# Optimization experiments

Hardware: AMD Instinct MI355X
Metric: run time of the kernel (lower is better)

The kernel has to match this reference:

```python
import jax, jax.numpy as jnp
import numpy as np

B, T, C = 8, 2048, 1024
HEAD = 64
BLOCK = 2048  # block_size == max_size == ramp_size


def setup_inputs() -> dict:
    key = jax.random.key(0)
    kx, kq, kk, kv = jax.random.split(key, 4)
    x = jax.random.normal(kx, (B, T, C), dtype=jnp.float32)
    # torch Linear(n_embd, head_size, bias=False): store as (C, HEAD) for x @ W
    s = 1.0 / np.sqrt(C)
    Wq = jax.random.uniform(kq, (C, HEAD), dtype=jnp.float32, minval=-s, maxval=s)
    Wk = jax.random.uniform(kk, (C, HEAD), dtype=jnp.float32, minval=-s, maxval=s)
    Wv = jax.random.uniform(kv, (C, HEAD), dtype=jnp.float32, minval=-s, maxval=s)
    # adaptive_span current_val parameter, shape (1,1,1), init 0
    current_val = jnp.zeros((1, 1, 1), dtype=jnp.float32)
    return {"x": x, "Wq": Wq, "Wk": Wk, "Wv": Wv, "current_val": current_val}


def reference(x, Wq, Wk, Wv, current_val):
    Bb, Tt, Cc = x.shape
    q = x @ Wq  # (B,T,H)
    k = x @ Wk
    v = x @ Wv
    scale = 1.0 / jnp.sqrt(jnp.asarray(HEAD, dtype=x.dtype))
    scores = jnp.einsum('bth,bsh->bts', q, k) * scale  # (B,T,T)
    causal = jnp.tril(jnp.ones((Tt, Tt), dtype=bool))
    scores = jnp.where(causal, scores, -jnp.inf)
    w = jax.nn.softmax(scores, axis=-1)
    # adaptive span post-softmax mask (T == max_size here, so no slicing)
    template = jnp.linspace(1.0 - BLOCK, 0.0, BLOCK, dtype=x.dtype)  # (T,)
    span = template + current_val * BLOCK  # (1,1,T)
    span = jnp.clip(span / BLOCK + 1.0, 0.0, 1.0)
    w = w * span
    w = w / (w.sum(-1, keepdims=True) + 1e-8)
    # dropout p=0 (eval) -> identity
    out = jnp.einsum('bts,bsh->bth', w, v)  # (B,T,H)
    return out
```

## Files before the change

kernel.cpp:

```cpp
#include <hip/hip_runtime.h>
#include <hip/hip_bf16.h>

#define BSZ 8
#define T 2048
#define C 1024
#define H 64
#define M (BSZ*T)

typedef __attribute__((ext_vector_type(4))) float f32x4;
typedef __attribute__((ext_vector_type(8))) short bf16x8;
typedef __attribute__((ext_vector_type(4))) short s16x4;
typedef __attribute__((ext_vector_type(8))) short s16x8;

static __device__ __forceinline__ short f2bf(float f) {
  union { float f; unsigned u; } c; c.f = f;
  unsigned u = c.u;
  u = (u + 0x7fffu + ((u >> 16) & 1u)) >> 16;
  return (short)u;
}

__global__ __launch_bounds__(256) void k_wt(const float* __restrict__ Wq,
                                            const float* __restrict__ Wk,
                                            const float* __restrict__ Wv,
                                            short* __restrict__ wt) {
  int idx = blockIdx.x * 256 + threadIdx.x;
  int c = idx & (C - 1);
  int n = idx >> 10;
  int w = n >> 6;
  int h = n & (H - 1);
  const float* W = (w == 0) ? Wq : (w == 1) ? Wk : Wv;
  wt[idx] = f2bf(W[c * H + h]);
}

__global__ __launch_bounds__(256) void k_qkv(const float* __restrict__ x,
                                             const short* __restrict__ wt,
                                             short* __restrict__ qb,
                                             short* __restrict__ kb,
                                             short* __restrict__ vt) {
  __shared__ short xs[2][32 * 64];
  __shared__ short wl[2][192 * 64];
  const int tid = threadIdx.x;
  const int m0 = blockIdx.x * 32;
  const int lane = tid & 63;
  const int wid = tid >> 6;
  const int g16 = lane >> 4, l16 = lane & 15;
  const int row0 = (wid & 1) * 16;
  const int nc0 = (wid >> 1) * 96;

  f32x4 acc[6];
  #pragma unroll
  for (int i = 0; i < 6; ++i) acc[i] = (f32x4){0.f, 0.f, 0.f, 0.f};

  const int xr = tid >> 4;
  const int xc4 = (tid & 15) * 4;
  const int xsw = xc4 ^ ((xr & 7) << 3);
  const int wr = tid >> 3;
  const int wc8 = (tid & 7) * 8;
  const int wsw = wc8 ^ ((wr & 7) << 3);
  const int fsw = (l16 & 7) << 3;

  float4 xA0, xA1, xB0, xB1;
  s16x8 wA0, wA1, wA2, wA3, wA4, wA5;
  s16x8 wB0, wB1, wB2, wB3, wB4, wB5;

#define QKV_LOAD(S, kc) do { \
    x##S##0 = *(const float4*)&x[(size_t)(m0 + xr) * C + (kc) + xc4]; \
    x##S##1 = *(const float4*)&x[(size_t)(m0 + xr + 16) * C + (kc) + xc4]; \
    w##S##0 = *(const s16x8*)&wt[(wr +   0) * C + (kc) + wc8]; \
    w##S##1 = *(const s16x8*)&wt[(wr +  32) * C + (kc) + wc8]; \
    w##S##2 = *(const s16x8*)&wt[(wr +  64) * C + (kc) + wc8]; \
    w##S##3 = *(const s16x8*)&wt[(wr +  96) * C + (kc) + wc8]; \
    w##S##4 = *(const s16x8*)&wt[(wr + 128) * C + (kc) + wc8]; \
    w##S##5 = *(const s16x8*)&wt[(wr + 160) * C + (kc) + wc8]; \
  } while (0)

#define QKV_STORE(S, buf) do { \
    s16x4 h0 = { f2bf((x##S##0).x), f2bf((x##S##0).y), f2bf((x##S##0).z), f2bf((x##S##0).w) }; \
    s16x4 h1 = { f2bf((x##S##1).x), f2bf((x##S##1).y), f2bf((x##S##1).z), f2bf((x##S##1).w) }; \
    *(s16x4*)&xs[buf][xr * 64 + xsw] = h0; \
    *(s16x4*)&xs[buf][(xr + 16) * 64 + xsw] = h1; \
    *(s16x8*)&wl[buf][(wr +   0) * 64 + wsw] = w##S##0; \
    *(s16x8*)&wl[buf][(wr +  32) * 64 + wsw] = w##S##1; \
    *(s16x8*)&wl[buf][(wr +  64) * 64 + wsw] = w##S##2; \
    *(s16x8*)&wl[buf][(wr +  96) * 64 + wsw] = w##S##3; \
    *(s16x8*)&wl[buf][(wr + 128) * 64 + wsw] = w##S##4; \
    *(s16x8*)&wl[buf][(wr + 160) * 64 + wsw] = w##S##5; \
  } while (0)

#define QKV_COMPUTE(buf) do { \
    _Pragma("unroll") \
    for (int ks = 0; ks < 2; ++ks) { \
      bf16x8 a = *(const bf16x8*)&xs[buf][(row0 + l16) * 64 + ((ks * 32 + g16 * 8) ^ fsw)]; \
      _Pragma("unroll") \
      for (int nt = 0; nt < 6; ++nt) { \
        bf16x8 bfr = *(const bf16x8*)&wl[buf][(nc0 + nt * 16 + l16) * 64 + ((ks * 32 + g16 * 8) ^ fsw)]; \
        acc[nt] = __builtin_amdgcn_mfma_f32_16x16x32_bf16(a, bfr, acc[nt], 0, 0, 0); \
      } \
    } \
  } while (0)

  QKV_LOAD(A, 0);
  QKV_STORE(A, 0);
  QKV_LOAD(B, 64);
  __syncthreads();

  #pragma unroll 1
  for (int ii = 0; ii < 8; ++ii) {
    if (ii < 7) QKV_LOAD(A, (2 * ii + 2) * 64);
    QKV_STORE(B, 1);
    QKV_COMPUTE(0);
    __syncthreads();
    if (ii < 7) {
      QKV_LOAD(B, (2 * ii + 3) * 64);
      QKV_STORE(A, 0);
    }
    QKV_COMPUTE(1);
    if (ii < 7) __syncthreads();
  }
#undef QKV_LOAD
#undef QKV_STORE
#undef QKV_COMPUTE

  const int r0 = row0 + g16 * 4;
  #pragma unroll
  for (int nt = 0; nt < 6; ++nt) {
    const int nglob = nc0 + nt * 16;
    const int which = nglob >> 6;
    const int col = (nglob & 63) + l16;
    #pragma unroll
    for (int j = 0; j < 4; ++j) {
      const int tg = m0 + r0 + j;
      const short val = f2bf(acc[nt][j]);
      if (which == 0)      qb[tg * H + col] = val;
      else if (which == 1) kb[tg * H + col] = val;
      else {
        const int b = tg >> 11, tl = tg & (T - 1);
        vt[((b << 6) + col) * T + tl] = val;
      }
    }
  }
}

__global__ __launch_bounds__(512, 4) void k_attn(const short* __restrict__ qb,
                                                 const short* __restrict__ kb,
                                                 const short* __restrict__ vt,
                                                 const float* __restrict__ cvp,
                                                 float* __restrict__ out) {
  __shared__ __align__(16) char smem[34816];
  short (*plds)[2][16][40] = (short (*)[2][16][40])smem;
  float (*Ow)[16][68]      = (float (*)[16][68])smem;
  __shared__ float mw[8][16];
  __shared__ float Lw[8][16];
  const int pid = blockIdx.x;
  const int b = pid & 7;
  const int pr = pid >> 3;
  const int tA = pr, tB = 127 - pr;
  const int q0A = tA << 4, q0B = tB << 4;
  const int nitA = (q0A + 47) >> 5;
  const int nitB = (q0B + 47) >> 5;
  const int NT = nitA + nitB;
  int wA = (8 * nitA + (NT >> 1)) / NT;
  wA = wA < 1 ? 1 : (wA > 7 ? 7 : wA);

  const int tid = threadIdx.x;
  const int wid = tid >> 6;
  const int lane = tid & 63;
  const int g16 = lane >> 4, l16 = lane & 15;
  const float cv = cvp[0];
  const float SCL = 0.125f * 1.44269504f;

  const bool onA = (wid < wA);
  const int q0 = onA ? q0A : q0B;
  const int nitW = onA ? nitA : nitB;
  const int nwt = onA ? wA : 8 - wA;
  const int wg = onA ? wid : wid - wA;
  const int npw = (nitW + nwt - 1) / nwt;
  const int lo = wg * npw;
  const int hi = (lo + npw < nitW) ? lo + npw : nitW;

  const short* qp = qb + ((size_t)(b << 11) + q0 + l16) * H + g16 * 8;
  bf16x8 qf0 = *(const bf16x8*)qp;
  bf16x8 qf1 = *(const bf16x8*)(qp + 32);
  const int qg = q0 + l16;

  float m = -3e38f, L = 0.f;
  f32x4 O[4];
  #pragma unroll
  for (int t4 = 0; t4 < 4; ++t4) O[t4] = (f32x4){0.f, 0.f, 0.f, 0.f};

  if (lo < hi) {
    const short* kp = kb + ((size_t)(b << 11) + lo * 32 + l16) * H + g16 * 8;
    const short* vp = vt + ((size_t)(b << 6) + l16) * T + lo * 32 + g16 * 8;
    bf16x8 kc0 = *(const bf16x8*)kp;
    bf16x8 kc1 = *(const bf16x8*)(kp + 32);
    bf16x8 kc2 = *(const bf16x8*)(kp + 16 * H);
    bf16x8 kc3 = *(const bf16x8*)(kp + 16 * H + 32);
    kp += 32 * H;

    for (int it = lo; it < hi; ++it) {
      bf16x8 kn0, kn1, kn2, kn3;
      const bool more = (it + 1 < hi);
      if (more) {
        kn0 = *(const bf16x8*)kp;
        kn1 = *(const bf16x8*)(kp + 32);
        kn2 = *(const bf16x8*)(kp + 16 * H);
        kn3 = *(const bf16x8*)(kp + 16 * H + 32);
      }
      bf16x8 v0 = *(const bf16x8*)vp;
      bf16x8 v1 = *(const bf16x8*)(vp + 16 * T);
      bf16x8 v2 = *(const bf16x8*)(vp + 32 * T);
      bf16x8 v3 = *(const bf16x8*)(vp + 48 * T);

      f32x4 s0 = {0.f,0.f,0.f,0.f}, s1 = {0.f,0.f,0.f,0.f};
      s0 = __builtin_amdgcn_mfma_f32_16x16x32_bf16(kc0, qf0, s0, 0, 0, 0);
      s0 = __builtin_amdgcn_mfma_f32_16x16x32_bf16(kc1, qf1, s0, 0, 0, 0);
      s1 = __builtin_amdgcn_mfma_f32_16x16x32_bf16(kc2, qf0, s1, 0, 0, 0);
      s1 = __builtin_amdgcn_mfma_f32_16x16x32_bf16(kc3, qf1, s1, 0, 0, 0);

      const int kv0 = it << 5;
      const int kvb = kv0 + g16 * 4;
      const bool diag = (kv0 + 31 > q0);
      float sv[8];
      if (diag) {
        #pragma unroll
        for (int r = 0; r < 8; ++r) {
          const int kvg = kvb + ((r >> 2) << 4) + (r & 3);
          const float s = ((r < 4) ? s0[r] : s1[r - 4]) * SCL;
          sv[r] = (kvg <= qg) ? s : -1e30f;
        }
      } else {
        #pragma unroll
        for (int r = 0; r < 8; ++r)
          sv[r] = ((r < 4) ? s0[r] : s1[r - 4]) * SCL;
      }

      float pmax = fmaxf(fmaxf(fmaxf(sv[0], sv[1]), fmaxf(sv[2], sv[3])),
                         fmaxf(fmaxf(sv[4], sv[5]), fmaxf(sv[6], sv[7])));
      if (!__all(pmax <= m + 7.f)) {
        float v = pmax;
        v = fmaxf(v, __shfl_xor(v, 16, 64));
        v = fmaxf(v, __shfl_xor(v, 32, 64));
        const float mn = fmaxf(m, v);
        const float al = exp2f(m - mn);
        m = mn;
        L *= al;
        #pragma unroll
        for (int t4 = 0; t4 < 4; ++t4) O[t4] *= al;
      }

      float p[8];
      #pragma unroll
      for (int r = 0; r < 8; ++r) {
        const int kvg = kvb + ((r >> 2) << 4) + (r & 3);
        const float sp = fminf(fmaxf((float)(kvg + 1) * (1.f / 2048.f) + cv, 0.f), 1.f);
        p[r] = exp2f(sv[r] - m) * sp;
      }
      if (diag) {
        #pragma unroll
        for (int r = 0; r < 8; ++r) {
          const int kvg = kvb + ((r >> 2) << 4) + (r & 3);
          p[r] = (kvg <= qg) ? p[r] : 0.f;
        }
      }
      L += ((p[0] + p[1]) + (p[2] + p[3])) + ((p[4] + p[5]) + (p[6] + p[7]));

      short (*pl)[40] = plds[wid][it & 1];
      #pragma unroll
      for (int r = 0; r < 8; r += 2) {
        union { float f; unsigned u; } a0, a1;
        a0.f = p[r]; a1.f = p[r + 1];
        const unsigned pk = (a0.u >> 16) | (a1.u & 0xffff0000u);
        *(unsigned*)&pl[l16][((r >> 2) << 4) + g16 * 4 + (r & 3)] = pk;
      }
      bf16x8 pa = *(const bf16x8*)&pl[l16][g16 * 8];
      O[0] = __builtin_amdgcn_mfma_f32_16x16x32_bf16(v0, pa, O[0], 0, 0, 0);
      O[1] = __builtin_amdgcn_mfma_f32_16x16x32_bf16(v1, pa, O[1], 0, 0, 0);
      O[2] = __builtin_amdgcn_mfma_f32_16x16x32_bf16(v2, pa, O[2], 0, 0, 0);
      O[3] = __builtin_amdgcn_mfma_f32_16x16x32_bf16(v3, pa, O[3], 0, 0, 0);

      if (more) { kc0 = kn0; kc1 = kn1; kc2 = kn2; kc3 = kn3; }
      kp += 32 * H;
      vp += 32;
    }
  }

  __syncthreads();

  float Lr = L;
  Lr += __shfl_xor(Lr, 16, 64);
  Lr += __shfl_xor(Lr, 32, 64);
  if (g16 == 0) { mw[wid][l16] = m; Lw[wid][l16] = Lr; }
  #pragma unroll
  for (int t4 = 0; t4 < 4; ++t4)
    *(f32x4*)&Ow[wid][l16][t4 * 16 + g16 * 4] = O[t4];
  __syncthreads();

  {
    const int r32 = tid >> 4;
    const int c4 = (tid & 15) << 2;
    const bool rowA = (r32 < 16);
    const int r = rowA ? r32 : r32 - 16;
    const int w0 = rowA ? 0 : wA;
    const int w1 = rowA ? wA : 8;
    const int q0r = rowA ? q0A : q0B;
    float Mx = -3e38f;
    for (int w = w0; w < w1; ++w) Mx = fmaxf(Mx, mw[w][r]);
    float Ls = 0.f;
    f32x4 o = (f32x4){0.f, 0.f, 0.f, 0.f};
    for (int w = w0; w < w1; ++w) {
      const float fw = exp2f(mw[w][r] - Mx);
      Ls += Lw[w][r] * fw;
      f32x4 ow = *(const f32x4*)&Ow[w][r][c4];
      o += ow * fw;
    }
    o *= 1.f / (Ls + 1e-30f);
    *(f32x4*)&out[(size_t)((b << 11) + q0r + r) * H + c4] = o;
  }
}

extern "C" void kernel_launch(void* const* d_in, const int* in_sizes, int n_in,
                              void* d_out, int out_size, void* d_ws, size_t ws_size,
                              hipStream_t stream) {
  const float* x  = (const float*)d_in[0];
  const float* Wq = (const float*)d_in[1];
  const float* Wk = (const float*)d_in[2];
  const float* Wv = (const float*)d_in[3];
  const float* cv = (const float*)d_in[4];
  float* out = (float*)d_out;

  char* ws = (char*)d_ws;
  short* qb = (short*)(ws);
  short* kb = (short*)(ws + (size_t)M * H * 2);
  short* vt = (short*)(ws + (size_t)2 * M * H * 2);
  short* wt = (short*)(ws + (size_t)3 * M * H * 2);

  hipLaunchKernelGGL(k_wt, dim3(3 * H * C / 256), dim3(256), 0, stream, Wq, Wk, Wv, wt);
  hipLaunchKernelGGL(k_qkv, dim3(M / 32), dim3(256), 0, stream, x, wt, qb, kb, vt);
  hipLaunchKernelGGL(k_attn, dim3(BSZ * T / 32), dim3(512), 0, stream, qb, kb, vt, cv, out);
}
```

Before: 63.40 us.

## Software-pipeline QK MFMA one step ahead and exchange P via ds_bpermute

The attention loop is restructured so the QK^T MFMAs for the next key block run while the current block's softmax and PV MFMAs execute. K loads are double-buffered two steps ahead using an unrolled ping-pong lambda. The P tile is now moved from the score layout to the MFMA operand layout with ds_bpermute lane shuffles instead of an LDS round-trip, which also removes the shared P buffer and a __syncthreads. Launch bounds drop from 4 to 2 waves-per-EU, allowing more registers for the extra live state at the cost of possible occupancy.

```diff
diff --git a/kernel.cpp b/kernel.cpp
--- a/kernel.cpp
+++ b/kernel.cpp
@@ -141,21 +141,18 @@
   }
 }
 
-__global__ __launch_bounds__(512, 4) void k_attn(const short* __restrict__ qb,
+__global__ __launch_bounds__(512, 2) void k_attn(const short* __restrict__ qb,
                                                  const short* __restrict__ kb,
                                                  const short* __restrict__ vt,
                                                  const float* __restrict__ cvp,
                                                  float* __restrict__ out) {
-  __shared__ __align__(16) char smem[34816];
-  short (*plds)[2][16][40] = (short (*)[2][16][40])smem;
-  float (*Ow)[16][68]      = (float (*)[16][68])smem;
+  __shared__ float Ow[8][16][68];
   __shared__ float mw[8][16];
   __shared__ float Lw[8][16];
   const int pid = blockIdx.x;
   const int b = pid & 7;
   const int pr = pid >> 3;
-  const int tA = pr, tB = 127 - pr;
-  const int q0A = tA << 4, q0B = tB << 4;
+  const int q0A = pr << 4, q0B = (127 - pr) << 4;
   const int nitA = (q0A + 47) >> 5;
   const int nitB = (q0B + 47) >> 5;
   const int NT = nitA + nitB;
@@ -183,6 +180,11 @@
   bf16x8 qf1 = *(const bf16x8*)(qp + 32);
   const int qg = q0 + l16;
 
+  const int gsel = (g16 & 1) << 5;
+  const int addrA = (gsel + l16) << 2;
+  const int addrB = (gsel + 16 + l16) << 2;
+  const bool ghi = (g16 >= 2);
+
   float m = -3e38f, L = 0.f;
   f32x4 O[4];
   #pragma unroll
@@ -191,31 +193,46 @@
   if (lo < hi) {
     const short* kp = kb + ((size_t)(b << 11) + lo * 32 + l16) * H + g16 * 8;
     const short* vp = vt + ((size_t)(b << 6) + l16) * T + lo * 32 + g16 * 8;
-    bf16x8 kc0 = *(const bf16x8*)kp;
-    bf16x8 kc1 = *(const bf16x8*)(kp + 32);
-    bf16x8 kc2 = *(const bf16x8*)(kp + 16 * H);
-    bf16x8 kc3 = *(const bf16x8*)(kp + 16 * H + 32);
+    bf16x8 kA0 = *(const bf16x8*)kp;
+    bf16x8 kA1 = *(const bf16x8*)(kp + 32);
+    bf16x8 kA2 = *(const bf16x8*)(kp + 16 * H);
+    bf16x8 kA3 = *(const bf16x8*)(kp + 16 * H + 32);
     kp += 32 * H;
-
-    for (int it = lo; it < hi; ++it) {
-      bf16x8 kn0, kn1, kn2, kn3;
-      const bool more = (it + 1 < hi);
-      if (more) {
-        kn0 = *(const bf16x8*)kp;
-        kn1 = *(const bf16x8*)(kp + 32);
-        kn2 = *(const bf16x8*)(kp + 16 * H);
-        kn3 = *(const bf16x8*)(kp + 16 * H + 32);
-      }
+    bf16x8 kB0 = kA0, kB1 = kA1, kB2 = kA2, kB3 = kA3;
+    if (lo + 1 < hi) {
+      kB0 = *(const bf16x8*)kp;
+      kB1 = *(const bf16x8*)(kp + 32);
+      kB2 = *(const bf16x8*)(kp + 16 * H);
+      kB3 = *(const bf16x8*)(kp + 16 * H + 32);
+      kp += 32 * H;
+    }
+    f32x4 s0c = {0.f,0.f,0.f,0.f}, s1c = {0.f,0.f,0.f,0.f};
+    s0c = __builtin_amdgcn_mfma_f32_16x16x32_bf16(kA0, qf0, s0c, 0, 0, 0);
+    s0c = __builtin_amdgcn_mfma_f32_16x16x32_bf16(kA1, qf1, s0c, 0, 0, 0);
+    s1c = __builtin_amdgcn_mfma_f32_16x16x32_bf16(kA2, qf0, s1c, 0, 0, 0);
+    s1c = __builtin_amdgcn_mfma_f32_16x16x32_bf16(kA3, qf1, s1c, 0, 0, 0);
+
+    auto astep = [&](int it,
+                     bf16x8 kn0, bf16x8 kn1, bf16x8 kn2, bf16x8 kn3,
+                     bf16x8& kl0, bf16x8& kl1, bf16x8& kl2, bf16x8& kl3) {
       bf16x8 v0 = *(const bf16x8*)vp;
       bf16x8 v1 = *(const bf16x8*)(vp + 16 * T);
       bf16x8 v2 = *(const bf16x8*)(vp + 32 * T);
       bf16x8 v3 = *(const bf16x8*)(vp + 48 * T);
-
-      f32x4 s0 = {0.f,0.f,0.f,0.f}, s1 = {0.f,0.f,0.f,0.f};
-      s0 = __builtin_amdgcn_mfma_f32_16x16x32_bf16(kc0, qf0, s0, 0, 0, 0);
-      s0 = __builtin_amdgcn_mfma_f32_16x16x32_bf16(kc1, qf1, s0, 0, 0, 0);
-      s1 = __builtin_amdgcn_mfma_f32_16x16x32_bf16(kc2, qf0, s1, 0, 0, 0);
-      s1 = __builtin_amdgcn_mfma_f32_16x16x32_bf16(kc3, qf1, s1, 0, 0, 0);
+      if (it + 2 < hi) {
+        kl0 = *(const bf16x8*)kp;
+        kl1 = *(const bf16x8*)(kp + 32);
+        kl2 = *(const bf16x8*)(kp + 16 * H);
+        kl3 = *(const bf16x8*)(kp + 16 * H + 32);
+        kp += 32 * H;
+      }
+      f32x4 n0 = {0.f,0.f,0.f,0.f}, n1 = {0.f,0.f,0.f,0.f};
+      if (it + 1 < hi) {
+        n0 = __builtin_amdgcn_mfma_f32_16x16x32_bf16(kn0, qf0, n0, 0, 0, 0);
+        n0 = __builtin_amdgcn_mfma_f32_16x16x32_bf16(kn1, qf1, n0, 0, 0, 0);
+        n1 = __builtin_amdgcn_mfma_f32_16x16x32_bf16(kn2, qf0, n1, 0, 0, 0);
+        n1 = __builtin_amdgcn_mfma_f32_16x16x32_bf16(kn3, qf1, n1, 0, 0, 0);
+      }
 
       const int kv0 = it << 5;
       const int kvb = kv0 + g16 * 4;
@@ -225,15 +242,14 @@
         #pragma unroll
         for (int r = 0; r < 8; ++r) {
           const int kvg = kvb + ((r >> 2) << 4) + (r & 3);
-          const float s = ((r < 4) ? s0[r] : s1[r - 4]) * SCL;
+          const float s = ((r < 4) ? s0c[r] : s1c[r - 4]) * SCL;
           sv[r] = (kvg <= qg) ? s : -1e30f;
         }
       } else {
         #pragma unroll
         for (int r = 0; r < 8; ++r)
-          sv[r] = ((r < 4) ? s0[r] : s1[r - 4]) * SCL;
-      }
-
+          sv[r] = ((r < 4) ? s0c[r] : s1c[r - 4]) * SCL;
+      }
       float pmax = fmaxf(fmaxf(fmaxf(sv[0], sv[1]), fmaxf(sv[2], sv[3])),
                          fmaxf(fmaxf(sv[4], sv[5]), fmaxf(sv[6], sv[7])));
       if (!__all(pmax <= m + 7.f)) {
@@ -247,7 +263,6 @@
         #pragma unroll
         for (int t4 = 0; t4 < 4; ++t4) O[t4] *= al;
       }
-
       float p[8];
       #pragma unroll
       for (int r = 0; r < 8; ++r) {
@@ -264,27 +279,43 @@
       }
       L += ((p[0] + p[1]) + (p[2] + p[3])) + ((p[4] + p[5]) + (p[6] + p[7]));
 
-      short (*pl)[40] = plds[wid][it & 1];
-      #pragma unroll
-      for (int r = 0; r < 8; r += 2) {
-        union { float f; unsigned u; } a0, a1;
-        a0.f = p[r]; a1.f = p[r + 1];
-        const unsigned pk = (a0.u >> 16) | (a1.u & 0xffff0000u);
-        *(unsigned*)&pl[l16][((r >> 2) << 4) + g16 * 4 + (r & 3)] = pk;
-      }
-      bf16x8 pa = *(const bf16x8*)&pl[l16][g16 * 8];
+      union { float f; unsigned u; } a0, a1;
+      unsigned d0, d1, d2, d3;
+      a0.f = p[0]; a1.f = p[1]; d0 = (a0.u >> 16) | (a1.u & 0xffff0000u);
+      a0.f = p[2]; a1.f = p[3]; d1 = (a0.u >> 16) | (a1.u & 0xffff0000u);
+      a0.f = p[4]; a1.f = p[5]; d2 = (a0.u >> 16) | (a1.u & 0xffff0000u);
+      a0.f = p[6]; a1.f = p[7]; d3 = (a0.u >> 16) | (a1.u & 0xffff0000u);
+      const int lo0 = __builtin_amdgcn_ds_bpermute(addrA, (int)d0);
+      const int lo1 = __builtin_amdgcn_ds_bpermute(addrA, (int)d1);
+      const int lo2 = __builtin_amdgcn_ds_bpermute(addrB, (int)d0);
+      const int lo3 = __builtin_amdgcn_ds_bpermute(addrB, (int)d1);
+      const int hi0 = __builtin_amdgcn_ds_bpermute(addrA, (int)d2);
+      const int hi1 = __builtin_amdgcn_ds_bpermute(addrA, (int)d3);
+      const int hi2 = __builtin_amdgcn_ds_bpermute(addrB, (int)d2);
+      const int hi3 = __builtin_amdgcn_ds_bpermute(addrB, (int)d3);
+      union { int w[4]; bf16x8 v8; } pu;
+      pu.w[0] = ghi ? hi0 : lo0;
+      pu.w[1] = ghi ? hi1 : lo1;
+      pu.w[2] = ghi ? hi2 : lo2;
+      pu.w[3] = ghi ? hi3 : lo3;
+      const bf16x8 pa = pu.v8;
+
       O[0] = __builtin_amdgcn_mfma_f32_16x16x32_bf16(v0, pa, O[0], 0, 0, 0);
       O[1] = __builtin_amdgcn_mfma_f32_16x16x32_bf16(v1, pa, O[1], 0, 0, 0);
       O[2] = __builtin_amdgcn_mfma_f32_16x16x32_bf16(v2, pa, O[2], 0, 0, 0);
       O[3] = __builtin_amdgcn_mfma_f32_16x16x32_bf16(v3, pa, O[3], 0, 0, 0);
 
-      if (more) { kc0 = kn0; kc1 = kn1; kc2 = kn2; kc3 = kn3; }
-      kp += 32 * H;
+      s0c = n0; s1c = n1;
       vp += 32;
+    };
+
+    #pragma unroll 1
+    for (int itb = lo; itb < hi; itb += 2) {
+      astep(itb, kB0, kB1, kB2, kB3, kA0, kA1, kA2, kA3);
+      if (itb + 1 < hi)
+        astep(itb + 1, kA0, kA1, kA2, kA3, kB0, kB1, kB2, kB3);
     }
   }
-
-  __syncthreads();
 
   float Lr = L;
   Lr += __shfl_xor(Lr, 16, 64);
```

Result: slower. 64.96 us (+2.5%).

## Process two KV tiles per iteration, bpermute P transpose, raw v_exp

Applied to the files above, without the earlier changes.

Unrolls the attention inner loop to handle two 32-key tiles per iteration with deeper K prefetch, interleaving their MFMAs for more independent work. Replaces the LDS store/load round trip for the P matrix with ds_bpermute lane shuffles, removing the shared P buffer and the barrier before the reduction. Uses raw v_exp_f32 instead of exp2f, and lowers the launch-bounds occupancy hint from 4 to 2 to allow more registers. The trade is higher register pressure and lower occupancy, plus more shuffle instructions.

```diff
diff --git a/kernel.cpp b/kernel.cpp
--- a/kernel.cpp
+++ b/kernel.cpp
@@ -17,6 +17,12 @@
   unsigned u = c.u;
   u = (u + 0x7fffu + ((u >> 16) & 1u)) >> 16;
   return (short)u;
+}
+
+static __device__ __forceinline__ float fexp2(float x) {
+  float r;
+  asm("v_exp_f32 %0, %1" : "=v"(r) : "v"(x));
+  return r;
 }
 
 __global__ __launch_bounds__(256) void k_wt(const float* __restrict__ Wq,
@@ -141,21 +147,18 @@
   }
 }
 
-__global__ __launch_bounds__(512, 4) void k_attn(const short* __restrict__ qb,
+__global__ __launch_bounds__(512, 2) void k_attn(const short* __restrict__ qb,
                                                  const short* __restrict__ kb,
                                                  const short* __restrict__ vt,
                                                  const float* __restrict__ cvp,
                                                  float* __restrict__ out) {
-  __shared__ __align__(16) char smem[34816];
-  short (*plds)[2][16][40] = (short (*)[2][16][40])smem;
-  float (*Ow)[16][68]      = (float (*)[16][68])smem;
+  __shared__ float Ow[8][16][68];
   __shared__ float mw[8][16];
   __shared__ float Lw[8][16];
   const int pid = blockIdx.x;
   const int b = pid & 7;
   const int pr = pid >> 3;
-  const int tA = pr, tB = 127 - pr;
-  const int q0A = tA << 4, q0B = tB << 4;
+  const int q0A = pr << 4, q0B = (127 - pr) << 4;
   const int nitA = (q0A + 47) >> 5;
   const int nitB = (q0B + 47) >> 5;
   const int NT = nitA + nitB;
@@ -183,6 +186,11 @@
   bf16x8 qf1 = *(const bf16x8*)(qp + 32);
   const int qg = q0 + l16;
 
+  const int gsel = (g16 & 1) << 5;
+  const int addrA = (gsel + l16) << 2;
+  const int addrB = (gsel + 16 + l16) << 2;
+  const bool ghi = (g16 >= 2);
+
   float m = -3e38f, L = 0.f;
   f32x4 O[4];
   #pragma unroll
@@ -191,100 +199,192 @@
   if (lo < hi) {
     const short* kp = kb + ((size_t)(b << 11) + lo * 32 + l16) * H + g16 * 8;
     const short* vp = vt + ((size_t)(b << 6) + l16) * T + lo * 32 + g16 * 8;
-    bf16x8 kc0 = *(const bf16x8*)kp;
-    bf16x8 kc1 = *(const bf16x8*)(kp + 32);
-    bf16x8 kc2 = *(const bf16x8*)(kp + 16 * H);
-    bf16x8 kc3 = *(const bf16x8*)(kp + 16 * H + 32);
+    bf16x8 k00 = *(const bf16x8*)kp;
+    bf16x8 k01 = *(const bf16x8*)(kp + 32);
+    bf16x8 k02 = *(const bf16x8*)(kp + 16 * H);
+    bf16x8 k03 = *(const bf16x8*)(kp + 16 * H + 32);
     kp += 32 * H;
-
-    for (int it = lo; it < hi; ++it) {
-      bf16x8 kn0, kn1, kn2, kn3;
-      const bool more = (it + 1 < hi);
-      if (more) {
-        kn0 = *(const bf16x8*)kp;
-        kn1 = *(const bf16x8*)(kp + 32);
-        kn2 = *(const bf16x8*)(kp + 16 * H);
-        kn3 = *(const bf16x8*)(kp + 16 * H + 32);
-      }
-      bf16x8 v0 = *(const bf16x8*)vp;
-      bf16x8 v1 = *(const bf16x8*)(vp + 16 * T);
-      bf16x8 v2 = *(const bf16x8*)(vp + 32 * T);
-      bf16x8 v3 = *(const bf16x8*)(vp + 48 * T);
-
-      f32x4 s0 = {0.f,0.f,0.f,0.f}, s1 = {0.f,0.f,0.f,0.f};
-      s0 = __builtin_amdgcn_mfma_f32_16x16x32_bf16(kc0, qf0, s0, 0, 0, 0);
-      s0 = __builtin_amdgcn_mfma_f32_16x16x32_bf16(kc1, qf1, s0, 0, 0, 0);
-      s1 = __builtin_amdgcn_mfma_f32_16x16x32_bf16(kc2, qf0, s1, 0, 0, 0);
-      s1 = __builtin_amdgcn_mfma_f32_16x16x32_bf16(kc3, qf1, s1, 0, 0, 0);
-
-      const int kv0 = it << 5;
-      const int kvb = kv0 + g16 * 4;
-      const bool diag = (kv0 + 31 > q0);
-      float sv[8];
-      if (diag) {
+    bf16x8 k10 = k00, k11 = k01, k12 = k02, k13 = k03;
+    if (lo + 1 < hi) {
+      k10 = *(const bf16x8*)kp;
+      k11 = *(const bf16x8*)(kp + 32);
+      k12 = *(const bf16x8*)(kp + 16 * H);
+      k13 = *(const bf16x8*)(kp + 16 * H + 32);
+      kp += 32 * H;
+    }
+
+    #pragma unroll 1
+    for (int it = lo; it < hi; it += 2) {
+      const bool has2 = (it + 1 < hi);
+      bf16x8 vA0 = *(const bf16x8*)vp;
+      bf16x8 vA1 = *(const bf16x8*)(vp + 16 * T);
+      bf16x8 vA2 = *(const bf16x8*)(vp + 32 * T);
+      bf16x8 vA3 = *(const bf16x8*)(vp + 48 * T);
+      bf16x8 vB0 = vA0, vB1 = vA1, vB2 = vA2, vB3 = vA3;
+      if (has2) {
+        vB0 = *(const bf16x8*)(vp + 32);
+        vB1 = *(const bf16x8*)(vp + 16 * T + 32);
+        vB2 = *(const bf16x8*)(vp + 32 * T + 32);
+        vB3 = *(const bf16x8*)(vp + 48 * T + 32);
+      }
+      bf16x8 n00, n01, n02, n03, n10, n11, n12, n13;
+      const bool pf0 = (it + 2 < hi), pf1 = (it + 3 < hi);
+      if (pf0) {
+        n00 = *(const bf16x8*)kp;
+        n01 = *(const bf16x8*)(kp + 32);
+        n02 = *(const bf16x8*)(kp + 16 * H);
+        n03 = *(const bf16x8*)(kp + 16 * H + 32);
+        kp += 32 * H;
+      }
+      if (pf1) {
+        n10 = *(const bf16x8*)kp;
+        n11 = *(const bf16x8*)(kp + 32);
+        n12 = *(const bf16x8*)(kp + 16 * H);
+        n13 = *(const bf16x8*)(kp + 16 * H + 32);
+        kp += 32 * H;
+      }
+
+      f32x4 sA0 = {0.f,0.f,0.f,0.f}, sA1 = {0.f,0.f,0.f,0.f};
+      f32x4 sB0 = {0.f,0.f,0.f,0.f}, sB1 = {0.f,0.f,0.f,0.f};
+      sA0 = __builtin_amdgcn_mfma_f32_16x16x32_bf16(k00, qf0, sA0, 0, 0, 0);
+      sB0 = __builtin_amdgcn_mfma_f32_16x16x32_bf16(k10, qf0, sB0, 0, 0, 0);
+      sA1 = __builtin_amdgcn_mfma_f32_16x16x32_bf16(k02, qf0, sA1, 0, 0, 0);
+      sB1 = __builtin_amdgcn_mfma_f32_16x16x32_bf16(k12, qf0, sB1, 0, 0, 0);
+      sA0 = __builtin_amdgcn_mfma_f32_16x16x32_bf16(k01, qf1, sA0, 0, 0, 0);
+      sB0 = __builtin_amdgcn_mfma_f32_16x16x32_bf16(k11, qf1, sB0, 0, 0, 0);
+      sA1 = __builtin_amdgcn_mfma_f32_16x16x32_bf16(k03, qf1, sA1, 0, 0, 0);
+      sB1 = __builtin_amdgcn_mfma_f32_16x16x32_bf16(k13, qf1, sB1, 0, 0, 0);
+
+      const int kv0A = it << 5, kv0B = kv0A + 32;
+      const int kvbA = kv0A + g16 * 4, kvbB = kv0B + g16 * 4;
+      const bool diagA = (kv0A + 31 > q0);
+      float svA[8], svB[8];
+      if (diagA) {
         #pragma unroll
         for (int r = 0; r < 8; ++r) {
-          const int kvg = kvb + ((r >> 2) << 4) + (r & 3);
-          const float s = ((r < 4) ? s0[r] : s1[r - 4]) * SCL;
-          sv[r] = (kvg <= qg) ? s : -1e30f;
+          const int kvg = kvbA + ((r >> 2) << 4) + (r & 3);
+          const float s = ((r < 4) ? sA0[r] : sA1[r - 4]) * SCL;
+          svA[r] = (kvg <= qg) ? s : -1e30f;
         }
       } else {
         #pragma unroll
         for (int r = 0; r < 8; ++r)
-          sv[r] = ((r < 4) ? s0[r] : s1[r - 4]) * SCL;
-      }
-
-      float pmax = fmaxf(fmaxf(fmaxf(sv[0], sv[1]), fmaxf(sv[2], sv[3])),
-                         fmaxf(fmaxf(sv[4], sv[5]), fmaxf(sv[6], sv[7])));
+          svA[r] = ((r < 4) ? sA0[r] : sA1[r - 4]) * SCL;
+      }
+      if (has2) {
+        const bool diagB = (kv0B + 31 > q0);
+        if (diagB) {
+          #pragma unroll
+          for (int r = 0; r < 8; ++r) {
+            const int kvg = kvbB + ((r >> 2) << 4) + (r & 3);
+            const float s = ((r < 4) ? sB0[r] : sB1[r - 4]) * SCL;
+            svB[r] = (kvg <= qg) ? s : -1e30f;
+          }
+        } else {
+          #pragma unroll
+          for (int r = 0; r < 8; ++r)
+            svB[r] = ((r < 4) ? sB0[r] : sB1[r - 4]) * SCL;
+        }
+      } else {
+        #pragma unroll
+        for (int r = 0; r < 8; ++r) svB[r] = -1e30f;
+      }
+
+      float pmax = -3e38f;
+      #pragma unroll
+      for (int r = 0; r < 8; ++r) pmax = fmaxf(pmax, fmaxf(svA[r], svB[r]));
       if (!__all(pmax <= m + 7.f)) {
         float v = pmax;
         v = fmaxf(v, __shfl_xor(v, 16, 64));
         v = fmaxf(v, __shfl_xor(v, 32, 64));
         const float mn = fmaxf(m, v);
-        const float al = exp2f(m - mn);
+        const float al = fexp2(m - mn);
         m = mn;
         L *= al;
         #pragma unroll
         for (int t4 = 0; t4 < 4; ++t4) O[t4] *= al;
       }
 
-      float p[8];
+      float pA[8], pB[8];
       #pragma unroll
       for (int r = 0; r < 8; ++r) {
-        const int kvg = kvb + ((r >> 2) << 4) + (r & 3);
-        const float sp = fminf(fmaxf((float)(kvg + 1) * (1.f / 2048.f) + cv, 0.f), 1.f);
-        p[r] = exp2f(sv[r] - m) * sp;
-      }
-      if (diag) {
+        const int kvgA = kvbA + ((r >> 2) << 4) + (r & 3);
+        const float spA = fminf(fmaxf((float)(kvgA + 1) * (1.f / 2048.f) + cv, 0.f), 1.f);
+        pA[r] = fexp2(svA[r] - m) * spA;
+        const float spB = fminf(fmaxf((float)(kvgA + 33) * (1.f / 2048.f) + cv, 0.f), 1.f);
+        pB[r] = fexp2(svB[r] - m) * spB;
+      }
+      if (diagA) {
         #pragma unroll
         for (int r = 0; r < 8; ++r) {
-          const int kvg = kvb + ((r >> 2) << 4) + (r & 3);
-          p[r] = (kvg <= qg) ? p[r] : 0.f;
+          const int kvg = kvbA + ((r >> 2) << 4) + (r & 3);
+          pA[r] = (kvg <= qg) ? pA[r] : 0.f;
+          pB[r] = (kvg + 32 <= qg) ? pB[r] : 0.f;
         }
-      }
-      L += ((p[0] + p[1]) + (p[2] + p[3])) + ((p[4] + p[5]) + (p[6] + p[7]));
-
-      short (*pl)[40] = plds[wid][it & 1];
-      #pragma unroll
-      for (int r = 0; r < 8; r += 2) {
-        union { float f; unsigned u; } a0, a1;
-        a0.f = p[r]; a1.f = p[r + 1];
-        const unsigned pk = (a0.u >> 16) | (a1.u & 0xffff0000u);
-        *(unsigned*)&pl[l16][((r >> 2) << 4) + g16 * 4 + (r & 3)] = pk;
-      }
-      bf16x8 pa = *(const bf16x8*)&pl[l16][g16 * 8];
-      O[0] = __builtin_amdgcn_mfma_f32_16x16x32_bf16(v0, pa, O[0], 0, 0, 0);
-      O[1] = __builtin_amdgcn_mfma_f32_16x16x32_bf16(v1, pa, O[1], 0, 0, 0);
-      O[2] = __builtin_amdgcn_mfma_f32_16x16x32_bf16(v2, pa, O[2], 0, 0, 0);
-      O[3] = __builtin_amdgcn_mfma_f32_16x16x32_bf16(v3, pa, O[3], 0, 0, 0);
-
-      if (more) { kc0 = kn0; kc1 = kn1; kc2 = kn2; kc3 = kn3; }
-      kp += 32 * H;
-      vp += 32;
+      } else if (kv0B + 31 > q0) {
+        #pragma unroll
+        for (int r = 0; r < 8; ++r) {
+          const int kvg = kvbB + ((r >> 2) << 4) + (r & 3);
+          pB[r] = (kvg <= qg) ? pB[r] : 0.f;
+        }
+      }
+      L += ((pA[0] + pA[1]) + (pA[2] + pA[3])) + ((pA[4] + pA[5]) + (pA[6] + pA[7]))
+         + ((pB[0] + pB[1]) + (pB[2] + pB[3])) + ((pB[4] + pB[5]) + (pB[6] + pB[7]));
+
+      union { float f; unsigned u; } a0, a1;
+      unsigned dA0, dA1, dA2, dA3, dB0, dB1, dB2, dB3;
+      a0.f = pA[0]; a1.f = pA[1]; dA0 = (a0.u >> 16) | (a1.u & 0xffff0000u);
+      a0.f = pA[2]; a1.f = pA[3]; dA1 = (a0.u >> 16) | (a1.u & 0xffff0000u);
+      a0.f = pA[4]; a1.f = pA[5]; dA2 = (a0.u >> 16) | (a1.u & 0xffff0000u);
+      a0.f = pA[6]; a1.f = pA[7]; dA3 = (a0.u >> 16) | (a1.u & 0xffff0000u);
+      a0.f = pB[0]; a1.f = pB[1]; dB0 = (a0.u >> 16) | (a1.u & 0xffff0000u);
+      a0.f = pB[2]; a1.f = pB[3]; dB1 = (a0.u >> 16) | (a1.u & 0xffff0000u);
+      a0.f = pB[4]; a1.f = pB[5]; dB2 = (a0.u >> 16) | (a1.u & 0xffff0000u);
+      a0.f = pB[6]; a1.f = pB[7]; dB3 = (a0.u >> 16) | (a1.u & 0xffff0000u);
+      const int Alo0 = __builtin_amdgcn_ds_bpermute(addrA, (int)dA0);
+      const int Alo1 = __builtin_amdgcn_ds_bpermute(addrA, (int)dA1);
+      const int Alo2 = __builtin_amdgcn_ds_bpermute(addrB, (int)dA0);
+      const int Alo3 = __builtin_amdgcn_ds_bpermute(addrB, (int)dA1);
+      const int Ahi0 = __builtin_amdgcn_ds_bpermute(addrA, (int)dA2);
+      const int Ahi1 = __builtin_amdgcn_ds_bpermute(addrA, (int)dA3);
+      const int Ahi2 = __builtin_amdgcn_ds_bpermute(addrB, (int)dA2);
+      const int Ahi3 = __builtin_amdgcn_ds_bpermute(addrB, (int)dA3);
+      const int Blo0 = __builtin_amdgcn_ds_bpermute(addrA, (int)dB0);
+      const int Blo1 = __builtin_amdgcn_ds_bpermute(addrA, (int)dB1);
+      const int Blo2 = __builtin_amdgcn_ds_bpermute(addrB, (int)dB0);
+      const int Blo3 = __builtin_amdgcn_ds_bpermute(addrB, (int)dB1);
+      const int Bhi0 = __builtin_amdgcn_ds_bpermute(addrA, (int)dB2);
+      const int Bhi1 = __builtin_amdgcn_ds_bpermute(addrA, (int)dB3);
+      const int Bhi2 = __builtin_amdgcn_ds_bpermute(addrB, (int)dB2);
+      const int Bhi3 = __builtin_amdgcn_ds_bpermute(addrB, (int)dB3);
+      union { int w[4]; bf16x8 v8; } puA, puB;
+      puA.w[0] = ghi ? Ahi0 : Alo0;
+      puA.w[1] = ghi ? Ahi1 : Alo1;
+      puA.w[2] = ghi ? Ahi2 : Alo2;
+      puA.w[3] = ghi ? Ahi3 : Alo3;
+      puB.w[0] = ghi ? Bhi0 : Blo0;
+      puB.w[1] = ghi ? Bhi1 : Blo1;
+      puB.w[2] = ghi ? Bhi2 : Blo2;
+      puB.w[3] = ghi ? Bhi3 : Blo3;
+      const bf16x8 paA = puA.v8;
+      const bf16x8 paB = puB.v8;
+
+      O[0] = __builtin_amdgcn_mfma_f32_16x16x32_bf16(vA0, paA, O[0], 0, 0, 0);
+      O[1] = __builtin_amdgcn_mfma_f32_16x16x32_bf16(vA1, paA, O[1], 0, 0, 0);
+      O[2] = __builtin_amdgcn_mfma_f32_16x16x32_bf16(vA2, paA, O[2], 0, 0, 0);
+      O[3] = __builtin_amdgcn_mfma_f32_16x16x32_bf16(vA3, paA, O[3], 0, 0, 0);
+      if (has2) {
+        O[0] = __builtin_amdgcn_mfma_f32_16x16x32_bf16(vB0, paB, O[0], 0, 0, 0);
+        O[1] = __builtin_amdgcn_mfma_f32_16x16x32_bf16(vB1, paB, O[1], 0, 0, 0);
+        O[2] = __builtin_amdgcn_mfma_f32_16x16x32_bf16(vB2, paB, O[2], 0, 0, 0);
+        O[3] = __builtin_amdgcn_mfma_f32_16x16x32_bf16(vB3, paB, O[3], 0, 0, 0);
+      }
+
+      if (pf0) { k00 = n00; k01 = n01; k02 = n02; k03 = n03; }
+      if (pf1) { k10 = n10; k11 = n11; k12 = n12; k13 = n13; }
+      vp += 64;
     }
   }
-
-  __syncthreads();
 
   float Lr = L;
   Lr += __shfl_xor(Lr, 16, 64);
@@ -308,7 +408,7 @@
     float Ls = 0.f;
     f32x4 o = (f32x4){0.f, 0.f, 0.f, 0.f};
     for (int w = w0; w < w1; ++w) {
-      const float fw = exp2f(mw[w][r] - Mx);
+      const float fw = fexp2(mw[w][r] - Mx);
       Ls += Lw[w][r] * fw;
       f32x4 ow = *(const f32x4*)&Ow[w][r][c4];
       o += ow * fw;
```

After: 66.31 us. 1.05x slower.
